# Performance work log

Hardware: AMD Instinct MI355X
Metric: run time of the kernel (lower is better)

The kernel has to match this reference:

```python
import jax, jax.numpy as jnp
import numpy as np

NEG = jnp.float32(-1e30)  # log-space -inf surrogate (safe for grads)


def _ctc_neg_log_likelihood(logprobs, labels, input_lens, label_lens):
    """CTC forward (alpha) recursion, blank=0.
    logprobs: (T, N, V) log-softmax outputs; labels: (N, L) int; lens: (N,).
    Returns per-sample negative log-likelihood (N,).
    """
    T, N, V = logprobs.shape
    L = labels.shape[1]
    S = 2 * L + 1
    # Extended label sequence: blank, l1, blank, l2, ..., blank
    z = jnp.zeros((N, S), dtype=labels.dtype).at[:, 1::2].set(labels)
    # Per-step emission log-probs for extended labels: (T, N, S)
    lp = logprobs[:, jnp.arange(N)[:, None], z]
    # Skip connection s-2 -> s allowed iff z[s] != blank and z[s] != z[s-2]
    z_m2 = jnp.pad(z, ((0, 0), (2, 0)))[:, :S]
    skip = (z != 0) & (z != z_m2)
    skip = skip.at[:, :2].set(False)

    alpha0 = jnp.full((N, S), NEG, dtype=logprobs.dtype)
    alpha0 = alpha0.at[:, 0].set(lp[0, :, 0]).at[:, 1].set(lp[0, :, 1])

    def step(alpha, xs):
        lp_t, t = xs
        a1 = jnp.pad(alpha, ((0, 0), (1, 0)), constant_values=NEG)[:, :S]
        a2 = jnp.pad(alpha, ((0, 0), (2, 0)), constant_values=NEG)[:, :S]
        a2 = jnp.where(skip, a2, NEG)
        new = jnp.logaddexp(jnp.logaddexp(alpha, a1), a2) + lp_t
        # Freeze alpha once past each sample's input length
        new = jnp.where((t < input_lens)[:, None], new, alpha)
        return new, None

    ts = jnp.arange(1, T)
    alpha, _ = jax.lax.scan(step, alpha0, (lp[1:], ts))

    idx_blank = (2 * label_lens).astype(jnp.int32)  # final blank position
    end1 = jnp.take_along_axis(alpha, idx_blank[:, None], axis=1)[:, 0]
    end2 = jnp.take_along_axis(alpha, (idx_blank - 1)[:, None], axis=1)[:, 0]
    return -jnp.logaddexp(end1, end2)


def setup_inputs() -> dict:
    key = jax.random.key(0)
    k1, k2, k3, k4, k5 = jax.random.split(key, 5)
    N, T, D, V, L = 16, 512, 512, 4096, 128
    encoder_out = jax.random.normal(k1, (N, T, D), dtype=jnp.float32)
    W = jax.random.normal(k2, (D, V), dtype=jnp.float32) / jnp.sqrt(jnp.float32(D))
    b = jnp.zeros((V,), dtype=jnp.float32)
    encoder_out_lens = jax.random.randint(k3, (N,), 300, T + 1, dtype=jnp.int32)
    padded_labels = jax.random.randint(k4, (N, L), 1, V, dtype=jnp.int32)
    label_lengths = jax.random.randint(k5, (N,), 64, L + 1, dtype=jnp.int32)
    return {
        "encoder_out": encoder_out,
        "W": W,
        "b": b,
        "encoder_out_lens": encoder_out_lens,
        "padded_labels": padded_labels,
        "label_lengths": label_lengths,
    }


def reference(encoder_out, W, b, encoder_out_lens, padded_labels, label_lengths):
    # Dropout is identity in eval mode. proj -> (N, T, V)
    logits = jnp.einsum("ntd,dv->ntv", encoder_out, W) + b
    # transpose(0,1).log_softmax(2) -> (T, N, V)
    logprobs = jax.nn.log_softmax(logits.transpose(1, 0, 2), axis=2)
    nll = _ctc_neg_log_likelihood(logprobs, padded_labels, encoder_out_lens, label_lengths)
    # reduction='sum', then divided by batch size
    return jnp.sum(nll) / padded_labels.shape[0]
```

## Files before the change

kernel.cpp:

```cpp
#include <hip/hip_runtime.h>

#define NEGF (-1e30f)

typedef __attribute__((ext_vector_type(8))) short bf16x8;
typedef __attribute__((ext_vector_type(4))) float f32x4;

__device__ __forceinline__ unsigned short f2bf(float x) {
  unsigned u = __float_as_uint(x);
  unsigned r = (u + 0x7FFFu + ((u >> 16) & 1u)) >> 16;
  return (unsigned short)r;
}


__device__ __forceinline__ void d_cvtx(int bid, int tid,
                                       const float* __restrict__ X,
                                       unsigned short* __restrict__ Xbf) {
  const int i = bid * 256 + tid;
  float4 v = ((const float4*)X)[i];
  ushort4 h;
  h.x = f2bf(v.x); h.y = f2bf(v.y); h.z = f2bf(v.z); h.w = f2bf(v.w);
  ((ushort4*)Xbf)[i] = h;
}

__device__ __forceinline__ void d_gather(int bid, int tid,
                                         const float* __restrict__ W,
                                         const float* __restrict__ b,
                                         const int* __restrict__ labels,
                                         float* __restrict__ Wgt,
                                         float* __restrict__ gb) {
  const int n  = bid >> 7;
  const int kc = bid & 127;
  const int k0 = kc << 2;
  for (int idx = tid; idx < 4 * 129; idx += 256) {
    const int kk = idx / 129;
    const int j  = idx - kk * 129;
    const int c  = (j == 0) ? 0 : labels[n * 128 + (j - 1)];
    const int k  = k0 + kk;
    Wgt[((size_t)(n * 512 + k)) * 132 + j] = W[(size_t)k * 4096 + c];
    if (kc == 0 && kk == 0) gb[n * 129 + j] = b[c];
  }
}

__device__ __forceinline__ void d_glp_raw(int bid, int tid, char* smem,
                                          const float* __restrict__ X,
                                          const float* __restrict__ Wgt,
                                          const float* __restrict__ gb,
                                          const int* __restrict__ lens,
                                          float* __restrict__ g) {
  const int n  = bid >> 4;
  const int t0 = (bid & 15) << 5;
  if (t0 >= lens[n]) return;
  const int m0 = n * 512 + t0;
  float (*xs)[512] = (float (*)[512])smem;
  {
    const float4* Xv = (const float4*)(X + (size_t)m0 * 512);
    float4* xsv = (float4*)(&xs[0][0]);
    for (int i = tid; i < 32 * 128; i += 256) xsv[i] = Xv[i];
  }
  __syncthreads();
  const int j = tid;
  if (j >= 129) return;
  const float* wp = Wgt + (size_t)(n * 512) * 132 + j;
  float acc[32];
#pragma unroll
  for (int r = 0; r < 32; ++r) acc[r] = 0.f;
  float w0 = wp[0], w1 = wp[132], w2 = wp[264], w3 = wp[396];
  for (int k4 = 0; k4 < 128; ++k4) {
    const int kn = (k4 + 1) & 127;
    float p0 = wp[(size_t)(kn * 4 + 0) * 132];
    float p1 = wp[(size_t)(kn * 4 + 1) * 132];
    float p2 = wp[(size_t)(kn * 4 + 2) * 132];
    float p3 = wp[(size_t)(kn * 4 + 3) * 132];
#pragma unroll
    for (int r = 0; r < 32; ++r) {
      float4 x4 = *(const float4*)(&xs[r][k4 << 2]);
      acc[r] = fmaf(x4.x, w0, acc[r]);
      acc[r] = fmaf(x4.y, w1, acc[r]);
      acc[r] = fmaf(x4.z, w2, acc[r]);
      acc[r] = fmaf(x4.w, w3, acc[r]);
    }
    w0 = p0; w1 = p1; w2 = p2; w3 = p3;
  }
  const float bb = gb[n * 129 + j];
#pragma unroll
  for (int r = 0; r < 32; ++r)
    g[(size_t)(m0 + r) * 132 + j] = acc[r] + bb;
}

__device__ __forceinline__ void d_wtrans(int bid, int tid, char* smem,
                                         const float* __restrict__ W,
                                         unsigned short* __restrict__ Wt) {
  float (*tile)[65] = (float (*)[65])smem;
  const int kb = bid & 7;
  const int vb = bid >> 3;
  const int k0 = kb << 6, v0 = vb << 6;
#pragma unroll
  for (int it = 0; it < 16; ++it) {
    const int idx = it * 256 + tid;
    const int r = idx >> 6, c = idx & 63;
    tile[r][c] = W[(size_t)(k0 + r) * 4096 + v0 + c];
  }
  __syncthreads();
#pragma unroll
  for (int it = 0; it < 16; ++it) {
    const int idx = it * 256 + tid;
    const int vr = idx >> 6, kc = idx & 63;
    Wt[(size_t)(v0 + vr) * 512 + k0 + kc] = f2bf(tile[kc][vr]);
  }
}

__device__ __forceinline__ void stage_tile(const unsigned short* __restrict__ src,
                                           int r0, char* ldsbase, int wave,
                                           int tid, int kbyte) {
#pragma unroll
  for (int j = 0; j < 2; ++j) {
    const int chunk = (tid & 3) ^ ((tid >> 3) & 3);
    const char* gp = (const char*)src +
        (size_t)(r0 + j * 64 + (tid >> 2)) * 1024 + kbyte + chunk * 16;
    char* lp = ldsbase + j * 4096 + wave * 1024;
    __builtin_amdgcn_global_load_lds(
        (const __attribute__((address_space(1))) unsigned int*)gp,
        (__attribute__((address_space(3))) unsigned int*)lp, 16, 0, 0);
  }
}

__device__ __forceinline__ void d_gemm(int gid, int tid, char* smem,
                                       const unsigned short* __restrict__ Xbf,
                                       const unsigned short* __restrict__ Wt,
                                       const float* __restrict__ bvec,
                                       const int* __restrict__ lens,
                                       float* __restrict__ pg) {
  const int bm = gid >> 5;
  const int bn = gid & 31;
  const int n  = bm >> 2;
  const int t0 = (bm & 3) << 7;
  if (t0 >= lens[n]) return;
  const int m0 = bm << 7;
  const int v0 = bn << 7;

  const int wave = tid >> 6;
  const int lane = tid & 63;
  const int lrow = lane & 15;
  const int lk   = (lane >> 4) * 16;
  const int lks  = lk ^ (((lrow >> 1) & 3) << 4);
  const int wr   = wave >> 1;
  const int wn   = wave & 1;

  f32x4 acc[4][4];
#pragma unroll
  for (int mi = 0; mi < 4; ++mi)
#pragma unroll
    for (int ni = 0; ni < 4; ++ni) acc[mi][ni] = (f32x4){0.f, 0.f, 0.f, 0.f};

  {
    char* buf = smem;
    stage_tile(Xbf, m0, buf + 0,    wave, tid, 0);
    stage_tile(Wt,  v0, buf + 8192, wave, tid, 0);
  }
  __syncthreads();

  int cur = 0;
  for (int kk = 0; kk < 16; ++kk) {
    if (kk < 15) {
      char* nbuf = smem + (cur ^ 1) * 16384;
      const int kb = (kk + 1) << 6;
      stage_tile(Xbf, m0, nbuf + 0,    wave, tid, kb);
      stage_tile(Wt,  v0, nbuf + 8192, wave, tid, kb);
    }
    const char* buf = smem + cur * 16384;
    bf16x8 ah[4], bh[4];
#pragma unroll
    for (int mi = 0; mi < 4; ++mi) {
      const int off = (wr * 64 + mi * 16 + lrow) * 64 + lks;
      ah[mi] = *(const bf16x8*)(buf + off);
    }
#pragma unroll
    for (int ni = 0; ni < 4; ++ni) {
      const int off = (wn * 64 + ni * 16 + lrow) * 64 + lks;
      bh[ni] = *(const bf16x8*)(buf + 8192 + off);
    }
#pragma unroll
    for (int mi = 0; mi < 4; ++mi)
#pragma unroll
      for (int ni = 0; ni < 4; ++ni)
        acc[mi][ni] = __builtin_amdgcn_mfma_f32_16x16x32_bf16(ah[mi], bh[ni], acc[mi][ni], 0, 0, 0);
    __syncthreads();
    cur ^= 1;
  }

  const float lg2e = 1.4426950408889634f;
  float bias[4];
#pragma unroll
  for (int ni = 0; ni < 4; ++ni) bias[ni] = bvec[v0 + wn * 64 + ni * 16 + lrow];
  float* part = (float*)(smem + 32768);
#pragma unroll
  for (int mi = 0; mi < 4; ++mi)
#pragma unroll
    for (int reg = 0; reg < 4; ++reg) {
      float s = 0.f;
#pragma unroll
      for (int ni = 0; ni < 4; ++ni)
        s += exp2f((acc[mi][ni][reg] + bias[ni]) * lg2e);
#pragma unroll
      for (int msk = 1; msk < 16; msk <<= 1) s += __shfl_xor(s, msk);
      if (lrow == 0)
        part[(wr * 64 + mi * 16 + (lane >> 4) * 4 + reg) * 2 + wn] = s;
    }
  __syncthreads();
  if (tid < 128)
    pg[(size_t)(m0 + tid) * 32 + bn] = part[tid * 2 + 0] + part[tid * 2 + 1];
}

__device__ __forceinline__ float lae3(float x, float y, float z) {
  float m = fmaxf(fmaxf(x, y), z);
  float e = __expf(x - m) + __expf(y - m) + __expf(z - m);
  return m + __logf(e);
}

__device__ __forceinline__ void stage32(const float* __restrict__ gsrc,
                                        char* ldsbase, int tid, int wave) {
#pragma unroll
  for (int k = 0; k < 4; ++k) {
    const char* gp = (const char*)gsrc + k * 4096 + (size_t)tid * 16;
    char* lp = ldsbase + k * 4096 + wave * 1024;
    __builtin_amdgcn_global_load_lds(
        (const __attribute__((address_space(1))) unsigned int*)gp,
        (__attribute__((address_space(3))) unsigned int*)lp, 16, 0, 0);
  }
  if (tid < 32) {
    const char* gp = (const char*)gsrc + 16384 + (size_t)tid * 16;
    char* lp = ldsbase + 16384;
    __builtin_amdgcn_global_load_lds(
        (const __attribute__((address_space(1))) unsigned int*)gp,
        (__attribute__((address_space(3))) unsigned int*)lp, 16, 0, 0);
  }
}

__device__ void d_scan(int sbid, int tid, char* smem,
                       const float* __restrict__ g,
                       const int* __restrict__ labels,
                       const int* __restrict__ in_lens,
                       const int* __restrict__ lab_lens,
                       float* __restrict__ af,
                       float* __restrict__ ab) {
  const int n    = sbid >> 1;
  const int dir  = sbid & 1;
  const int wave = tid >> 6;
  const int l    = tid & 63;
  const int len  = in_lens[n];
  const int tm   = len >> 1;
  const float* gn = g + (size_t)n * 512 * 132;
  const int s0 = 5 * l;

  int jm0, jm1, jm2, jm3, jm4;
  {
    int jmv[5];
#pragma unroll
    for (int i = 0; i < 5; ++i) {
      const int s = s0 + i;
      jmv[i] = (s < 257 && (s & 1)) ? ((s + 1) >> 1) : 0;
    }
    jm0 = jmv[0]; jm1 = jmv[1]; jm2 = jmv[2]; jm3 = jmv[3]; jm4 = jmv[4];
  }

  if (dir == 0) {
    bool sk0, sk1, sk2, sk3, sk4;
    {
      bool skv[5];
#pragma unroll
      for (int i = 0; i < 5; ++i) {
        const int s = s0 + i;
        skv[i] = false;
        if (s < 257 && (s & 1) && s >= 3) {
          const int li = (s - 1) >> 1;
          const int cl = labels[n * 128 + li];
          skv[i] = (cl != 0) && (cl != labels[n * 128 + li - 1]);
        }
      }
      sk0 = skv[0]; sk1 = skv[1]; sk2 = skv[2]; sk3 = skv[3]; sk4 = skv[4];
    }
    stage32(gn, smem, tid, wave);
    __syncthreads();

    float a0 = NEGF, a1 = NEGF, a2 = NEGF, a3 = NEGF, a4 = NEGF;
    if (tid < 64 && l == 0) {
      const float* B0 = (const float*)smem;
      a0 = B0[0]; a1 = B0[1];
    }
    float a3p = NEGF, a4p = NEGF;

    int t = 1, c = 0;
    while (true) {
      const bool more = ((c + 1) << 5) <= tm;
      if (more)
        stage32(gn + (size_t)((c + 1) << 5) * 132,
                smem + ((c + 1) & 1) * 16896, tid, wave);
      if (tid < 64) {
        const float* B = (const float*)(smem + (c & 1) * 16896);
        const int ce = (c << 5) + 31;
        const int tend = (tm < ce) ? tm : ce;
        int ro = (t - (c << 5)) * 132;
        float p0 = B[ro + jm0], p1 = B[ro + jm1], p2 = B[ro + jm2],
              p3 = B[ro + jm3], p4 = B[ro + jm4];
        for (; t <= tend; ++t) {
          const int ro2 = (t < tend) ? ro + 132 : ro;
          const float q0 = B[ro2 + jm0];
          const float q1 = B[ro2 + jm1];
          const float q2 = B[ro2 + jm2];
          const float q3 = B[ro2 + jm3];
          const float q4 = B[ro2 + jm4];
          float x3 = a3p, x4 = a4p;
          if (l == 0) { x3 = NEGF; x4 = NEGF; }
          const float n3 = lae3(a3, a2, sk3 ? a1 : NEGF) + p3;
          const float n4 = lae3(a4, a3, sk4 ? a2 : NEGF) + p4;
          a3p = __shfl_up(n3, 1);
          a4p = __shfl_up(n4, 1);
          const float n0 = lae3(a0, x4, sk0 ? x3 : NEGF) + p0;
          const float n1 = lae3(a1, a0, sk1 ? x4 : NEGF) + p1;
          const float n2 = lae3(a2, a1, sk2 ? a0 : NEGF) + p2;
          a0 = n0; a1 = n1; a2 = n2; a3 = n3; a4 = n4;
          p0 = q0; p1 = q1; p2 = q2; p3 = q3; p4 = q4;
          ro = ro2;
        }
      }
      if (!more) break;
      __syncthreads();
      ++c;
    }
    if (tid < 64) {
      float* o = af + n * 320 + s0;
      o[0] = a0; o[1] = a1; o[2] = a2; o[3] = a3; o[4] = a4;
    }
  } else {
    bool skd0, skd1, skd2, skd3, skd4;
    {
      bool skv[5];
#pragma unroll
      for (int i = 0; i < 5; ++i) {
        const int s2 = s0 + i + 2;
        skv[i] = false;
        if (s2 < 257 && (s2 & 1) && s2 >= 3) {
          const int li = (s2 - 1) >> 1;
          const int cl = labels[n * 128 + li];
          skv[i] = (cl != 0) && (cl != labels[n * 128 + li - 1]);
        }
      }
      skd0 = skv[0]; skd1 = skv[1]; skd2 = skv[2]; skd3 = skv[3]; skd4 = skv[4];
    }
    int c = (len - 1) >> 5;
    stage32(gn + (size_t)(c << 5) * 132, smem + (c & 1) * 16896, tid, wave);
    __syncthreads();

    float b0, b1, b2, b3, b4;
    {
      const int ll = lab_lens[n];
      const int i1 = 2 * ll, i2 = 2 * ll - 1;
      b0 = (s0 + 0 == i1 || s0 + 0 == i2) ? 0.f : NEGF;
      b1 = (s0 + 1 == i1 || s0 + 1 == i2) ? 0.f : NEGF;
      b2 = (s0 + 2 == i1 || s0 + 2 == i2) ? 0.f : NEGF;
      b3 = (s0 + 3 == i1 || s0 + 3 == i2) ? 0.f : NEGF;
      b4 = (s0 + 4 == i1 || s0 + 4 == i2) ? 0.f : NEGF;
    }

    int t = len - 2;
    while (true) {
      const bool more = (c << 5) > tm + 1;
      if (more)
        stage32(gn + (size_t)((c - 1) << 5) * 132,
                smem + ((c - 1) & 1) * 16896, tid, wave);
      if (tid < 64) {
        const float* B = (const float*)(smem + (c & 1) * 16896);
        const int cl0 = (c << 5) - 1;
        const int tlo = (tm > cl0) ? tm : cl0;
        int ro = (t + 1 - (c << 5)) * 132;
        float p0 = B[ro + jm0], p1 = B[ro + jm1], p2 = B[ro + jm2],
              p3 = B[ro + jm3], p4 = B[ro + jm4];
        for (; t >= tlo; --t) {
          const int ro2 = (t - 1 >= tlo) ? ro - 132 : ro;
          const float q0 = B[ro2 + jm0];
          const float q1 = B[ro2 + jm1];
          const float q2 = B[ro2 + jm2];
          const float q3 = B[ro2 + jm3];
          const float q4 = B[ro2 + jm4];
          const float c0 = b0 + p0;
          const float c1 = b1 + p1;
          float c5 = __shfl_down(c0, 1);
          float c6 = __shfl_down(c1, 1);
          const float c2 = b2 + p2;
          const float c3 = b3 + p3;
          const float c4 = b4 + p4;
          const float m0n = lae3(c0, c1, skd0 ? c2 : NEGF);
          const float m1n = lae3(c1, c2, skd1 ? c3 : NEGF);
          const float m2n = lae3(c2, c3, skd2 ? c4 : NEGF);
          if (l == 63) { c5 = NEGF; c6 = NEGF; }
          const float m3n = lae3(c3, c4, skd3 ? c5 : NEGF);
          const float m4n = lae3(c4, c5, skd4 ? c6 : NEGF);
          b0 = m0n; b1 = m1n; b2 = m2n; b3 = m3n; b4 = m4n;
          p0 = q0; p1 = q1; p2 = q2; p3 = q3; p4 = q4;
          ro = ro2;
        }
      }
      if (!more) break;
      __syncthreads();
      --c;
    }
    if (tid < 64) {
      float* o = ab + n * 320 + s0;
      o[0] = b0; o[1] = b1; o[2] = b2; o[3] = b3; o[4] = b4;
    }
  }
}


__global__ __launch_bounds__(256) void k_prep1(const float* __restrict__ X,
                                               unsigned short* __restrict__ Xbf,
                                               const float* __restrict__ W,
                                               const float* __restrict__ b,
                                               const int* __restrict__ labels,
                                               float* __restrict__ Wgt,
                                               float* __restrict__ gb) {
  const int bid = blockIdx.x;
  if (bid < 4096) d_cvtx(bid, threadIdx.x, X, Xbf);
  else            d_gather(bid - 4096, threadIdx.x, W, b, labels, Wgt, gb);
}

__global__ __launch_bounds__(256) void k_prep2(const float* __restrict__ X,
                                               const float* __restrict__ Wgt,
                                               const float* __restrict__ gb,
                                               const int* __restrict__ lens,
                                               float* __restrict__ g,
                                               const float* __restrict__ W,
                                               unsigned short* __restrict__ Wt) {
  __shared__ __align__(16) char smem[65536];
  const int bid = blockIdx.x;
  if (bid < 256) d_glp_raw(bid, threadIdx.x, smem, X, Wgt, gb, lens, g);
  else           d_wtrans(bid - 256, threadIdx.x, smem, W, Wt);
}

__global__ __launch_bounds__(256, 4) void k_main(const float* __restrict__ g,
                                                 const int* __restrict__ labels,
                                                 const int* __restrict__ in_lens,
                                                 const int* __restrict__ lab_lens,
                                                 float* __restrict__ af,
                                                 float* __restrict__ ab,
                                                 const unsigned short* __restrict__ Xbf,
                                                 const unsigned short* __restrict__ Wt,
                                                 const float* __restrict__ bvec,
                                                 float* __restrict__ pg) {
  __shared__ __align__(16) char smem[33792];
  const int bid = blockIdx.x;
  if (bid < 32) d_scan(bid, threadIdx.x, smem, g, labels, in_lens, lab_lens, af, ab);
  else          d_gemm(bid - 32, threadIdx.x, smem, Xbf, Wt, bvec, in_lens, pg);
}

__global__ __launch_bounds__(256) void k_lsered(const float* __restrict__ pg,
                                                const int* __restrict__ lens,
                                                double* __restrict__ Sn) {
  const int n = blockIdx.x, tid = threadIdx.x;
  const int len = lens[n];
  __shared__ double red[256];
  double s = 0.0;
  for (int t = tid; t < len; t += 256) {
    const float4* p = (const float4*)(pg + ((size_t)(n * 512 + t)) * 32);
    float e = 0.f;
#pragma unroll
    for (int i = 0; i < 8; ++i) { float4 v = p[i]; e += v.x + v.y + v.z + v.w; }
    s += (double)__logf(e);
  }
  red[tid] = s;
  __syncthreads();
  for (int off = 128; off > 0; off >>= 1) {
    if (tid < off) red[tid] += red[tid + off];
    __syncthreads();
  }
  if (tid == 0) Sn[n] = red[0];
}

__global__ void k_comb(const float* __restrict__ af,
                       const float* __restrict__ ab,
                       const double* __restrict__ Sn,
                       float* __restrict__ nll) {
  const int n = blockIdx.x;
  const int l = threadIdx.x;
  const int s0 = 5 * l;
  float v0 = NEGF, v1 = NEGF, v2 = NEGF, v3 = NEGF, v4 = NEGF;
  const float* f = af + n * 320 + s0;
  const float* bb = ab + n * 320 + s0;
  if (s0 + 0 < 257) v0 = f[0] + bb[0];
  if (s0 + 1 < 257) v1 = f[1] + bb[1];
  if (s0 + 2 < 257) v2 = f[2] + bb[2];
  if (s0 + 3 < 257) v3 = f[3] + bb[3];
  if (s0 + 4 < 257) v4 = f[4] + bb[4];
  float M = fmaxf(fmaxf(v0, v1), fmaxf(fmaxf(v2, v3), v4));
#pragma unroll
  for (int off = 1; off < 64; off <<= 1) M = fmaxf(M, __shfl_xor(M, off));
  float e = __expf(v0 - M) + __expf(v1 - M) + __expf(v2 - M)
          + __expf(v3 - M) + __expf(v4 - M);
#pragma unroll
  for (int off = 1; off < 64; off <<= 1) e += __shfl_xor(e, off);
  if (l == 0) nll[n] = (float)(Sn[n] - (double)(M + __logf(e)));
}

__global__ void k_finish(const float* __restrict__ nll, float* __restrict__ out) {
  const int l = threadIdx.x;
  float v = (l < 16) ? nll[l] : 0.f;
#pragma unroll
  for (int off = 8; off > 0; off >>= 1) v += __shfl_down(v, off);
  if (l == 0) out[0] = v * 0.0625f;
}

__global__ void k_gather_w(const float* __restrict__ W,
                           const float* __restrict__ b,
                           const int* __restrict__ labels,
                           float* __restrict__ Wgt,
                           float* __restrict__ gb) {
  d_gather(blockIdx.x, threadIdx.x, W, b, labels, Wgt, gb);
}

__global__ __launch_bounds__(256) void k_glp(const float* __restrict__ X,
                                             const float* __restrict__ Wgt,
                                             const float* __restrict__ gb,
                                             const float* __restrict__ lse,
                                             const int* __restrict__ lens,
                                             float* __restrict__ g) {
  const int blk = blockIdx.x;
  const int n   = blk >> 4;
  const int t0  = (blk & 15) << 5;
  if (t0 >= lens[n]) return;
  const int m0 = n * 512 + t0;
  __shared__ float xs[32][512];
  {
    const float4* Xv = (const float4*)(X + (size_t)m0 * 512);
    float4* xsv = (float4*)(&xs[0][0]);
    for (int i = threadIdx.x; i < 32 * 128; i += 256) xsv[i] = Xv[i];
  }
  __syncthreads();
  const int j = threadIdx.x;
  if (j >= 129) return;
  const float* wp = Wgt + (size_t)(n * 512) * 132 + j;
  float acc[32];
#pragma unroll
  for (int r = 0; r < 32; ++r) acc[r] = 0.f;
  float w0 = wp[0], w1 = wp[132], w2 = wp[264], w3 = wp[396];
  for (int k4 = 0; k4 < 128; ++k4) {
    const int kn = (k4 + 1) & 127;
    float p0 = wp[(size_t)(kn * 4 + 0) * 132];
    float p1 = wp[(size_t)(kn * 4 + 1) * 132];
    float p2 = wp[(size_t)(kn * 4 + 2) * 132];
    float p3 = wp[(size_t)(kn * 4 + 3) * 132];
#pragma unroll
    for (int r = 0; r < 32; ++r) {
      float4 x4 = *(const float4*)(&xs[r][k4 << 2]);
      acc[r] = fmaf(x4.x, w0, acc[r]);
      acc[r] = fmaf(x4.y, w1, acc[r]);
      acc[r] = fmaf(x4.z, w2, acc[r]);
      acc[r] = fmaf(x4.w, w3, acc[r]);
    }
    w0 = p0; w1 = p1; w2 = p2; w3 = p3;
  }
  const float bb = gb[n * 129 + j];
#pragma unroll
  for (int r = 0; r < 32; ++r)
    g[(size_t)(m0 + r) * 132 + j] = acc[r] + bb - lse[m0 + r];
}

__global__ void k_ctc_g(const float* __restrict__ g,
                        const int* __restrict__ labels,
                        const int* __restrict__ in_lens,
                        const int* __restrict__ lab_lens,
                        float* __restrict__ nll) {
  const int n = blockIdx.x;
  const int l = threadIdx.x;
  const float* gn = g + (size_t)n * 512 * 132;
  const int len = in_lens[n];
  const int s0 = 5 * l;
  int jm[5]; bool sk[5];
#pragma unroll
  for (int i = 0; i < 5; ++i) {
    const int s = s0 + i;
    const bool valid = (s < 257);
    jm[i] = (valid && (s & 1)) ? ((s + 1) >> 1) : 0;
    sk[i] = false;
    if (valid && (s & 1) && s >= 3) {
      const int li = (s - 1) >> 1;
      const int cl = labels[n * 128 + li];
      sk[i] = (cl != 0) && (cl != labels[n * 128 + li - 1]);
    }
  }
  float a[5];
  a[0] = (l == 0) ? gn[0] : NEGF;
  a[1] = (l == 0) ? gn[1] : NEGF;
  a[2] = NEGF; a[3] = NEGF; a[4] = NEGF;
  float lp[5];
#pragma unroll
  for (int i = 0; i < 5; ++i) lp[i] = gn[132 + jm[i]];
  for (int t = 1; t < len; ++t) {
    const int tp = (t + 1 < len) ? (t + 1) : t;
    float np[5];
#pragma unroll
    for (int i = 0; i < 5; ++i) np[i] = gn[(size_t)tp * 132 + jm[i]];
    float a3p = __shfl_up(a[3], 1);
    float a4p = __shfl_up(a[4], 1);
    if (l == 0) { a3p = NEGF; a4p = NEGF; }
    const float b0 = lae3(a[0], a4p,  sk[0] ? a3p  : NEGF) + lp[0];
    const float b1 = lae3(a[1], a[0], sk[1] ? a4p  : NEGF) + lp[1];
    const float b2 = lae3(a[2], a[1], sk[2] ? a[0] : NEGF) + lp[2];
    const float b3 = lae3(a[3], a[2], sk[3] ? a[1] : NEGF) + lp[3];
    const float b4 = lae3(a[4], a[3], sk[4] ? a[2] : NEGF) + lp[4];
    a[0] = b0; a[1] = b1; a[2] = b2; a[3] = b3; a[4] = b4;
#pragma unroll
    for (int i = 0; i < 5; ++i) lp[i] = np[i];
  }
  __shared__ float al[320];
#pragma unroll
  for (int i = 0; i < 5; ++i) al[s0 + i] = a[i];
  __syncthreads();
  if (l == 0) {
    const int ll  = lab_lens[n];
    const int idx = 2 * ll;
    const float e1 = al[idx], e2 = al[idx - 1];
    const float m = fmaxf(e1, e2);
    const float r = m + __logf(__expf(e1 - m) + __expf(e2 - m));
    nll[n] = -r;
  }
}

__global__ __launch_bounds__(512, 2) void k_lse(const float* __restrict__ X,
                                                const float* __restrict__ W,
                                                const float* __restrict__ b,
                                                const int* __restrict__ lens,
                                                float* __restrict__ lse,
                                                float* __restrict__ red_g) {
  const int blk = blockIdx.x;
  const int n   = blk >> 4;
  const int t0  = (blk & 15) << 5;
  if (t0 >= lens[n]) return;
  const int m0 = n * 512 + t0;
  __shared__ float xs[32][512];
  {
    const float4* Xv = (const float4*)(X + (size_t)m0 * 512);
    float4* xsv = (float4*)(&xs[0][0]);
    for (int i = threadIdx.x; i < 32 * 128; i += 512) xsv[i] = Xv[i];
  }
  float* redb = red_g + (size_t)blk * 256;
  for (int i = threadIdx.x; i < 256; i += 512) redb[i] = 0.f;
  __syncthreads();
  const int wave = threadIdx.x >> 6;
  const int lane = threadIdx.x & 63;
  for (int j = 0; j < 4; ++j) {
    const int v = (j << 10) + (threadIdx.x << 1);
    const float* Wv = W + v;
    float2 acc[32];
#pragma unroll
    for (int r = 0; r < 32; ++r) acc[r] = make_float2(0.f, 0.f);
    float2 w0 = *(const float2*)(Wv + 0 * 4096);
    float2 w1 = *(const float2*)(Wv + 1 * 4096);
    float2 w2 = *(const float2*)(Wv + 2 * 4096);
    float2 w3 = *(const float2*)(Wv + 3 * 4096);
    for (int k4 = 0; k4 < 128; ++k4) {
      const int kn = (k4 + 1) & 127;
      float2 p0 = *(const float2*)(Wv + (kn * 4 + 0) * 4096);
      float2 p1 = *(const float2*)(Wv + (kn * 4 + 1) * 4096);
      float2 p2 = *(const float2*)(Wv + (kn * 4 + 2) * 4096);
      float2 p3 = *(const float2*)(Wv + (kn * 4 + 3) * 4096);
#pragma unroll
      for (int r = 0; r < 32; ++r) {
        float4 x4 = *(const float4*)(&xs[r][k4 << 2]);
        acc[r].x = fmaf(x4.x, w0.x, acc[r].x);
        acc[r].y = fmaf(x4.x, w0.y, acc[r].y);
        acc[r].x = fmaf(x4.y, w1.x, acc[r].x);
        acc[r].y = fmaf(x4.y, w1.y, acc[r].y);
        acc[r].x = fmaf(x4.z, w2.x, acc[r].x);
        acc[r].y = fmaf(x4.z, w2.y, acc[r].y);
        acc[r].x = fmaf(x4.w, w3.x, acc[r].x);
        acc[r].y = fmaf(x4.w, w3.y, acc[r].y);
      }
      w0 = p0; w1 = p1; w2 = p2; w3 = p3;
    }
    const float2 bb = *(const float2*)(b + v);
#pragma unroll
    for (int r = 0; r < 32; ++r) {
      float e = __expf(acc[r].x + bb.x) + __expf(acc[r].y + bb.y);
#pragma unroll
      for (int off = 32; off > 0; off >>= 1) e += __shfl_xor(e, off);
      if (lane == 0) redb[wave * 32 + r] += e;
    }
  }
  __syncthreads();
  if (threadIdx.x < 32) {
    float s = 0.f;
#pragma unroll
    for (int w = 0; w < 8; ++w) s += redb[w * 32 + threadIdx.x];
    lse[m0 + threadIdx.x] = __logf(s);
  }
}

__global__ void k_finish_neg(const float* __restrict__ nll, float* __restrict__ out) {
  const int l = threadIdx.x;
  float v = (l < 16) ? nll[l] : 0.f;
#pragma unroll
  for (int off = 8; off > 0; off >>= 1) v += __shfl_down(v, off);
  if (l == 0) out[0] = v * 0.0625f;
}

extern "C" void kernel_launch(void* const* d_in, const int* in_sizes, int n_in,
                              void* d_out, int out_size, void* d_ws, size_t ws_size,
                              hipStream_t stream) {
  const float* X        = (const float*)d_in[0];
  const float* W        = (const float*)d_in[1];
  const float* b        = (const float*)d_in[2];
  const int*   in_lens  = (const int*)d_in[3];
  const int*   labels   = (const int*)d_in[4];
  const int*   lab_lens = (const int*)d_in[5];
  float* out = (float*)d_out;
  char* wsb = (char*)d_ws;

  const size_t NEED = 34906240;
  if (ws_size >= NEED) {
    float* pg  = (float*)(wsb + 32768);
    float* Wgt = (float*)(wsb + 1081344);
    float* gb  = (float*)(wsb + 5406720);
    float* g   = (float*)(wsb + 5414976);
    float* nll = (float*)(wsb + 9740352);
    unsigned short* Xbf = (unsigned short*)(wsb + 9740416);
    unsigned short* Wt  = (unsigned short*)(wsb + 18129024);
    float*  af = (float*)(wsb + 26517632);
    float*  ab = (float*)(wsb + 26517632 + 20480);
    double* Sn = (double*)(wsb + 26517632 + 40960);

    k_prep1<<<dim3(6144), dim3(256), 0, stream>>>(X, Xbf, W, b, labels, Wgt, gb);
    k_prep2<<<dim3(768), dim3(256), 0, stream>>>(X, Wgt, gb, in_lens, g, W, Wt);
    k_main<<<dim3(2080), dim3(256), 0, stream>>>(g, labels, in_lens, lab_lens,
                                                 af, ab, Xbf, Wt, b, pg);
    k_lsered<<<dim3(16), dim3(256), 0, stream>>>(pg, in_lens, Sn);
    k_comb<<<dim3(16), dim3(64), 0, stream>>>(af, ab, Sn, nll);
    k_finish<<<dim3(1), dim3(64), 0, stream>>>(nll, out);
  } else {
    float* ws    = (float*)d_ws;
    float* lse   = ws;
    float* red_g = ws + 8192;
    float* Wgt   = ws + 8192 + 65536;
    float* gb    = Wgt + 1081344;
    float* g     = gb + 2064;
    float* nll   = g + 1081344;
    k_lse<<<dim3(256), dim3(512), 0, stream>>>(X, W, b, in_lens, lse, red_g);
    k_gather_w<<<dim3(2048), dim3(256), 0, stream>>>(W, b, labels, Wgt, gb);
    k_glp<<<dim3(256), dim3(256), 0, stream>>>(X, Wgt, gb, lse, in_lens, g);
    k_ctc_g<<<dim3(16), dim3(64), 0, stream>>>(g, labels, in_lens, lab_lens, nll);
    k_finish_neg<<<dim3(1), dim3(64), 0, stream>>>(nll, out);
  }
}
```

Baseline: 185.0 us.

## Run CTC scan in log2 domain, prioritize scan waves, fuse tail kernels

Pre-scales the gathered emission scores by log2(e) so the forward/backward CTC recursions use native exp2/log2 instead of natural exp/log, and converts back to natural log only at the end. It raises the wave priority of the serial scan blocks that share k_main with the GEMM blocks, to shorten the critical path. It also merges the LSE-reduction and combine kernels into a single tail kernel, removing one launch. The base-2 change alters rounding slightly, and the fallback path now calls k_finish in place of k_finish_neg.

```diff
diff --git a/kernel.cpp b/kernel.cpp
--- a/kernel.cpp
+++ b/kernel.cpp
@@ -1,6 +1,8 @@
 #include <hip/hip_runtime.h>
 
 #define NEGF (-1e30f)
+#define LOG2E 1.4426950408889634f
+#define LN2d  0.6931471805599453
 
 typedef __attribute__((ext_vector_type(8))) short bf16x8;
 typedef __attribute__((ext_vector_type(4))) float f32x4;
@@ -84,7 +86,7 @@
   const float bb = gb[n * 129 + j];
 #pragma unroll
   for (int r = 0; r < 32; ++r)
-    g[(size_t)(m0 + r) * 132 + j] = acc[r] + bb;
+    g[(size_t)(m0 + r) * 132 + j] = (acc[r] + bb) * LOG2E;
 }
 
 __device__ __forceinline__ void d_wtrans(int bid, int tid, char* smem,
@@ -188,7 +190,7 @@
     cur ^= 1;
   }
 
-  const float lg2e = 1.4426950408889634f;
+  const float lg2e = LOG2E;
   float bias[4];
 #pragma unroll
   for (int ni = 0; ni < 4; ++ni) bias[ni] = bvec[v0 + wn * 64 + ni * 16 + lrow];
@@ -211,7 +213,13 @@
     pg[(size_t)(m0 + tid) * 32 + bn] = part[tid * 2 + 0] + part[tid * 2 + 1];
 }
 
-__device__ __forceinline__ float lae3(float x, float y, float z) {
+__device__ __forceinline__ float lae32(float x, float y, float z) {
+  float m = fmaxf(fmaxf(x, y), z);
+  float e = exp2f(x - m) + exp2f(y - m) + exp2f(z - m);
+  return m + __log2f(e);
+}
+
+__device__ __forceinline__ float lae3n(float x, float y, float z) {
   float m = fmaxf(fmaxf(x, y), z);
   float e = __expf(x - m) + __expf(y - m) + __expf(z - m);
   return m + __logf(e);
@@ -311,13 +319,13 @@
           const float q4 = B[ro2 + jm4];
           float x3 = a3p, x4 = a4p;
           if (l == 0) { x3 = NEGF; x4 = NEGF; }
-          const float n3 = lae3(a3, a2, sk3 ? a1 : NEGF) + p3;
-          const float n4 = lae3(a4, a3, sk4 ? a2 : NEGF) + p4;
+          const float n3 = lae32(a3, a2, sk3 ? a1 : NEGF) + p3;
+          const float n4 = lae32(a4, a3, sk4 ? a2 : NEGF) + p4;
           a3p = __shfl_up(n3, 1);
           a4p = __shfl_up(n4, 1);
-          const float n0 = lae3(a0, x4, sk0 ? x3 : NEGF) + p0;
-          const float n1 = lae3(a1, a0, sk1 ? x4 : NEGF) + p1;
-          const float n2 = lae3(a2, a1, sk2 ? a0 : NEGF) + p2;
+          const float n0 = lae32(a0, x4, sk0 ? x3 : NEGF) + p0;
+          const float n1 = lae32(a1, a0, sk1 ? x4 : NEGF) + p1;
+          const float n2 = lae32(a2, a1, sk2 ? a0 : NEGF) + p2;
           a0 = n0; a1 = n1; a2 = n2; a3 = n3; a4 = n4;
           p0 = q0; p1 = q1; p2 = q2; p3 = q3; p4 = q4;
           ro = ro2;
@@ -389,12 +397,12 @@
           const float c2 = b2 + p2;
           const float c3 = b3 + p3;
           const float c4 = b4 + p4;
-          const float m0n = lae3(c0, c1, skd0 ? c2 : NEGF);
-          const float m1n = lae3(c1, c2, skd1 ? c3 : NEGF);
-          const float m2n = lae3(c2, c3, skd2 ? c4 : NEGF);
+          const float m0n = lae32(c0, c1, skd0 ? c2 : NEGF);
+          const float m1n = lae32(c1, c2, skd1 ? c3 : NEGF);
+          const float m2n = lae32(c2, c3, skd2 ? c4 : NEGF);
           if (l == 63) { c5 = NEGF; c6 = NEGF; }
-          const float m3n = lae3(c3, c4, skd3 ? c5 : NEGF);
-          const float m4n = lae3(c4, c5, skd4 ? c6 : NEGF);
+          const float m3n = lae32(c3, c4, skd3 ? c5 : NEGF);
+          const float m4n = lae32(c4, c5, skd4 ? c6 : NEGF);
           b0 = m0n; b1 = m1n; b2 = m2n; b3 = m3n; b4 = m4n;
           p0 = q0; p1 = q1; p2 = q2; p3 = q3; p4 = q4;
           ro = ro2;
@@ -449,13 +457,20 @@
                                                  float* __restrict__ pg) {
   __shared__ __align__(16) char smem[33792];
   const int bid = blockIdx.x;
-  if (bid < 32) d_scan(bid, threadIdx.x, smem, g, labels, in_lens, lab_lens, af, ab);
-  else          d_gemm(bid - 32, threadIdx.x, smem, Xbf, Wt, bvec, in_lens, pg);
-}
-
-__global__ __launch_bounds__(256) void k_lsered(const float* __restrict__ pg,
-                                                const int* __restrict__ lens,
-                                                double* __restrict__ Sn) {
+  if (bid < 32) {
+    __builtin_amdgcn_s_setprio(1);
+    d_scan(bid, threadIdx.x, smem, g, labels, in_lens, lab_lens, af, ab);
+    __builtin_amdgcn_s_setprio(0);
+  } else {
+    d_gemm(bid - 32, threadIdx.x, smem, Xbf, Wt, bvec, in_lens, pg);
+  }
+}
+
+__global__ __launch_bounds__(256) void k_tail(const float* __restrict__ pg,
+                                              const int* __restrict__ lens,
+                                              const float* __restrict__ af,
+                                              const float* __restrict__ ab,
+                                              float* __restrict__ nll) {
   const int n = blockIdx.x, tid = threadIdx.x;
   const int len = lens[n];
   __shared__ double red[256];
@@ -473,32 +488,27 @@
     if (tid < off) red[tid] += red[tid + off];
     __syncthreads();
   }
-  if (tid == 0) Sn[n] = red[0];
-}
-
-__global__ void k_comb(const float* __restrict__ af,
-                       const float* __restrict__ ab,
-                       const double* __restrict__ Sn,
-                       float* __restrict__ nll) {
-  const int n = blockIdx.x;
-  const int l = threadIdx.x;
-  const int s0 = 5 * l;
-  float v0 = NEGF, v1 = NEGF, v2 = NEGF, v3 = NEGF, v4 = NEGF;
-  const float* f = af + n * 320 + s0;
-  const float* bb = ab + n * 320 + s0;
-  if (s0 + 0 < 257) v0 = f[0] + bb[0];
-  if (s0 + 1 < 257) v1 = f[1] + bb[1];
-  if (s0 + 2 < 257) v2 = f[2] + bb[2];
-  if (s0 + 3 < 257) v3 = f[3] + bb[3];
-  if (s0 + 4 < 257) v4 = f[4] + bb[4];
-  float M = fmaxf(fmaxf(v0, v1), fmaxf(fmaxf(v2, v3), v4));
-#pragma unroll
-  for (int off = 1; off < 64; off <<= 1) M = fmaxf(M, __shfl_xor(M, off));
-  float e = __expf(v0 - M) + __expf(v1 - M) + __expf(v2 - M)
-          + __expf(v3 - M) + __expf(v4 - M);
-#pragma unroll
-  for (int off = 1; off < 64; off <<= 1) e += __shfl_xor(e, off);
-  if (l == 0) nll[n] = (float)(Sn[n] - (double)(M + __logf(e)));
+  if (tid < 64) {
+    const int l = tid;
+    const int s0 = 5 * l;
+    float v0 = NEGF, v1 = NEGF, v2 = NEGF, v3 = NEGF, v4 = NEGF;
+    const float* f = af + n * 320 + s0;
+    const float* bb = ab + n * 320 + s0;
+    if (s0 + 0 < 257) v0 = f[0] + bb[0];
+    if (s0 + 1 < 257) v1 = f[1] + bb[1];
+    if (s0 + 2 < 257) v2 = f[2] + bb[2];
+    if (s0 + 3 < 257) v3 = f[3] + bb[3];
+    if (s0 + 4 < 257) v4 = f[4] + bb[4];
+    float M = fmaxf(fmaxf(v0, v1), fmaxf(fmaxf(v2, v3), v4));
+#pragma unroll
+    for (int off = 1; off < 64; off <<= 1) M = fmaxf(M, __shfl_xor(M, off));
+    float e = exp2f(v0 - M) + exp2f(v1 - M) + exp2f(v2 - M)
+            + exp2f(v3 - M) + exp2f(v4 - M);
+#pragma unroll
+    for (int off = 1; off < 64; off <<= 1) e += __shfl_xor(e, off);
+    if (l == 0)
+      nll[n] = (float)(red[0] - (double)(M + __log2f(e)) * LN2d);
+  }
 }
 
 __global__ void k_finish(const float* __restrict__ nll, float* __restrict__ out) {
@@ -602,11 +612,11 @@
     float a3p = __shfl_up(a[3], 1);
     float a4p = __shfl_up(a[4], 1);
     if (l == 0) { a3p = NEGF; a4p = NEGF; }
-    const float b0 = lae3(a[0], a4p,  sk[0] ? a3p  : NEGF) + lp[0];
-    const float b1 = lae3(a[1], a[0], sk[1] ? a4p  : NEGF) + lp[1];
-    const float b2 = lae3(a[2], a[1], sk[2] ? a[0] : NEGF) + lp[2];
-    const float b3 = lae3(a[3], a[2], sk[3] ? a[1] : NEGF) + lp[3];
-    const float b4 = lae3(a[4], a[3], sk[4] ? a[2] : NEGF) + lp[4];
+    const float b0 = lae3n(a[0], a4p,  sk[0] ? a3p  : NEGF) + lp[0];
+    const float b1 = lae3n(a[1], a[0], sk[1] ? a4p  : NEGF) + lp[1];
+    const float b2 = lae3n(a[2], a[1], sk[2] ? a[0] : NEGF) + lp[2];
+    const float b3 = lae3n(a[3], a[2], sk[3] ? a[1] : NEGF) + lp[3];
+    const float b4 = lae3n(a[4], a[3], sk[4] ? a[2] : NEGF) + lp[4];
     a[0] = b0; a[1] = b1; a[2] = b2; a[3] = b3; a[4] = b4;
 #pragma unroll
     for (int i = 0; i < 5; ++i) lp[i] = np[i];
@@ -695,14 +705,6 @@
   }
 }
 
-__global__ void k_finish_neg(const float* __restrict__ nll, float* __restrict__ out) {
-  const int l = threadIdx.x;
-  float v = (l < 16) ? nll[l] : 0.f;
-#pragma unroll
-  for (int off = 8; off > 0; off >>= 1) v += __shfl_down(v, off);
-  if (l == 0) out[0] = v * 0.0625f;
-}
-
 extern "C" void kernel_launch(void* const* d_in, const int* in_sizes, int n_in,
                               void* d_out, int out_size, void* d_ws, size_t ws_size,
                               hipStream_t stream) {
@@ -724,16 +726,14 @@
     float* nll = (float*)(wsb + 9740352);
     unsigned short* Xbf = (unsigned short*)(wsb + 9740416);
     unsigned short* Wt  = (unsigned short*)(wsb + 18129024);
-    float*  af = (float*)(wsb + 26517632);
-    float*  ab = (float*)(wsb + 26517632 + 20480);
-    double* Sn = (double*)(wsb + 26517632 + 40960);
+    float* af = (float*)(wsb + 26517632);
+    float* ab = (float*)(wsb + 26517632 + 20480);
 
     k_prep1<<<dim3(6144), dim3(256), 0, stream>>>(X, Xbf, W, b, labels, Wgt, gb);
     k_prep2<<<dim3(768), dim3(256), 0, stream>>>(X, Wgt, gb, in_lens, g, W, Wt);
     k_main<<<dim3(2080), dim3(256), 0, stream>>>(g, labels, in_lens, lab_lens,
                                                  af, ab, Xbf, Wt, b, pg);
-    k_lsered<<<dim3(16), dim3(256), 0, stream>>>(pg, in_lens, Sn);
-    k_comb<<<dim3(16), dim3(64), 0, stream>>>(af, ab, Sn, nll);
+    k_tail<<<dim3(16), dim3(256), 0, stream>>>(pg, in_lens, af, ab, nll);
     k_finish<<<dim3(1), dim3(64), 0, stream>>>(nll, out);
   } else {
     float* ws    = (float*)d_ws;
@@ -747,6 +747,6 @@
     k_gather_w<<<dim3(2048), dim3(256), 0, stream>>>(W, b, labels, Wgt, gb);
     k_glp<<<dim3(256), dim3(256), 0, stream>>>(X, Wgt, gb, lse, in_lens, g);
     k_ctc_g<<<dim3(16), dim3(64), 0, stream>>>(g, labels, in_lens, lab_lens, nll);
-    k_finish_neg<<<dim3(1), dim3(64), 0, stream>>>(nll, out);
-  }
-}
+    k_finish<<<dim3(1), dim3(64), 0, stream>>>(nll, out);
+  }
+}
```

New measurement: 186.7 us. About the same (+0.9%).
